# Optimization experiments

Measured on AMD Instinct MI355X. Metric: run time of the kernel, lower is better.

## Reference

```python
import jax, jax.numpy as jnp
import numpy as np

TOTAL_NODES = 262144
NUM_GRAPHS = 1024
MAX_NODES = 512
D = 256


def setup_inputs() -> dict:
    key = jax.random.key(0)
    k1, k2 = jax.random.split(key)
    node_emb = jax.random.normal(k1, (TOTAL_NODES, D), dtype=jnp.float32)
    batch_idx = jnp.sort(jax.random.randint(k2, (TOTAL_NODES,), 0, NUM_GRAPHS, dtype=jnp.int64))
    return {"node_emb": node_emb, "batch_idx": batch_idx,
            "num_graphs": NUM_GRAPHS, "max_nodes": MAX_NODES}


def reference(node_emb, batch_idx, num_graphs, max_nodes):
    # counts[g] = number of nodes in graph g  (torch.bincount)
    n = node_emb.shape[0]
    counts = jax.ops.segment_sum(jnp.ones((n,), dtype=jnp.int32), batch_idx,
                                 num_segments=num_graphs)
    # exclusive prefix sum -> start offset of each graph's node block
    starts = jnp.cumsum(counts) - counts
    # position of each node within its graph (batch_idx is sorted)
    pos = jnp.arange(n, dtype=jnp.int32) - starts[batch_idx]
    # single fused scatter replacing the per-graph python loop
    enc_states = jnp.zeros((num_graphs, max_nodes, node_emb.shape[-1]),
                           dtype=node_emb.dtype)
    enc_states = enc_states.at[batch_idx, pos].set(node_emb)
    # mask: first counts[g] slots of each row are 1
    enc_mask = (jnp.arange(max_nodes, dtype=jnp.int32)[None, :]
                < counts[:, None]).astype(jnp.int32)
    return enc_states, enc_mask
```

## Files before the change

kernel.cpp:

```cpp
#include <hip/hip_runtime.h>

#define NUM_GRAPHS 1024
#define MAX_NODES  512
#define DIM        256
#define D4         (DIM / 4)

typedef float f4 __attribute__((ext_vector_type(4)));

__device__ __forceinline__ int lower_bound_idx(const int* __restrict__ b, int n,
                                               bool is64, int key) {
    int lo = 0, hi = n;
    while (lo < hi) {
        int mid = (lo + hi) >> 1;
        int v = is64 ? b[2 * mid] : b[mid];
        if (v < key) lo = mid + 1; else hi = mid;
    }
    return lo;
}

__global__ void __launch_bounds__(256)
scatter_states_kernel(const f4* __restrict__ emb,
                      const int* __restrict__ bidx32, int n,
                      f4* __restrict__ out, float* __restrict__ mask) {
    __shared__ int sc[2];
    const int g = blockIdx.x;

    if (threadIdx.x < 2) {
        const bool is64 = (bidx32[n - 1] == 0);
        sc[threadIdx.x] = lower_bound_idx(bidx32, n, is64, g + threadIdx.x);
    }
    __syncthreads();
    const int s = sc[0];
    const int c = sc[1] - sc[0];

    const int lane  = threadIdx.x & 63;
    const int w     = threadIdx.x >> 6;
    const int rbase = w * 128;

    const f4* wemb = emb + (size_t)(s + rbase) * D4 + lane;
    f4*       wout = out + ((size_t)g * MAX_NODES + rbase) * D4 + lane;

    int ncopy = c - rbase;
    ncopy = ncopy < 0 ? 0 : (ncopy > 128 ? 128 : ncopy);

    int it = 0;
#pragma unroll 8
    for (; it < ncopy; ++it)
        wout[it * D4] = wemb[it * D4];
    const f4 z = (f4)(0.f);
#pragma unroll 8
    for (; it < 128; ++it)
        wout[it * D4] = z;

    float* mg = mask + (size_t)g * MAX_NODES;
    mg[threadIdx.x]       = (threadIdx.x < c)       ? 1.0f : 0.0f;
    mg[256 + threadIdx.x] = (256 + (int)threadIdx.x < c) ? 1.0f : 0.0f;
}

extern "C" void kernel_launch(void* const* d_in, const int* in_sizes, int n_in,
                              void* d_out, int out_size, void* d_ws, size_t ws_size,
                              hipStream_t stream) {
    const float* node_emb = (const float*)d_in[0];
    const int*   bidx32   = (const int*)d_in[1];
    const int    n        = in_sizes[1];

    float* mask = (float*)d_out + (size_t)NUM_GRAPHS * MAX_NODES * DIM;
    scatter_states_kernel<<<NUM_GRAPHS, 256, 0, stream>>>(
        (const f4*)node_emb, bidx32, n, (f4*)d_out, mask);
}
```

Baseline: 173.5 us.

## Assign one wavefront per graph and compute segment bounds per wave

Each 64-lane wavefront now handles one whole graph (all 512 rows) instead of a block of four waves splitting rows. Each wave runs its own binary search, with lanes alternating between the start and end keys, and broadcasts the bounds via shuffles, removing the shared memory and block barrier. The grid shrinks to a quarter as many blocks. This cuts per-block synchronisation and serial search latency, but each wave now does a longer serial copy loop of 512 rows and the work per wave becomes less balanced.

```diff
diff --git a/kernel.cpp b/kernel.cpp
--- a/kernel.cpp
+++ b/kernel.cpp
@@ -7,54 +7,44 @@
 
 typedef float f4 __attribute__((ext_vector_type(4)));
 
-__device__ __forceinline__ int lower_bound_idx(const int* __restrict__ b, int n,
-                                               bool is64, int key) {
-    int lo = 0, hi = n;
-    while (lo < hi) {
-        int mid = (lo + hi) >> 1;
-        int v = is64 ? b[2 * mid] : b[mid];
-        if (v < key) lo = mid + 1; else hi = mid;
-    }
-    return lo;
-}
-
 __global__ void __launch_bounds__(256)
 scatter_states_kernel(const f4* __restrict__ emb,
                       const int* __restrict__ bidx32, int n,
                       f4* __restrict__ out, float* __restrict__ mask) {
-    __shared__ int sc[2];
-    const int g = blockIdx.x;
+    const int lane = threadIdx.x & 63;
+    const int g    = (blockIdx.x * blockDim.x + threadIdx.x) >> 6;
 
-    if (threadIdx.x < 2) {
-        const bool is64 = (bidx32[n - 1] == 0);
-        sc[threadIdx.x] = lower_bound_idx(bidx32, n, is64, g + threadIdx.x);
+    const bool is64 = (bidx32[n - 1] == 0);
+
+    const int key = g + (lane & 1);
+    int lo = 0, hi = n;
+    while (lo < hi) {
+        int mid = (lo + hi) >> 1;
+        int v = is64 ? bidx32[2 * mid] : bidx32[mid];
+        if (v < key) lo = mid + 1; else hi = mid;
     }
-    __syncthreads();
-    const int s = sc[0];
-    const int c = sc[1] - sc[0];
+    const int s = __shfl(lo, 0, 64);
+    const int e = __shfl(lo, 1, 64);
+    const int c = e - s;
 
-    const int lane  = threadIdx.x & 63;
-    const int w     = threadIdx.x >> 6;
-    const int rbase = w * 128;
-
-    const f4* wemb = emb + (size_t)(s + rbase) * D4 + lane;
-    f4*       wout = out + ((size_t)g * MAX_NODES + rbase) * D4 + lane;
-
-    int ncopy = c - rbase;
-    ncopy = ncopy < 0 ? 0 : (ncopy > 128 ? 128 : ncopy);
+    const f4* wemb = emb + (size_t)s * D4 + lane;
+    f4*       wout = out + (size_t)g * MAX_NODES * D4 + lane;
 
     int it = 0;
 #pragma unroll 8
-    for (; it < ncopy; ++it)
+    for (; it < c; ++it)
         wout[it * D4] = wemb[it * D4];
     const f4 z = (f4)(0.f);
 #pragma unroll 8
-    for (; it < 128; ++it)
+    for (; it < MAX_NODES; ++it)
         wout[it * D4] = z;
 
     float* mg = mask + (size_t)g * MAX_NODES;
-    mg[threadIdx.x]       = (threadIdx.x < c)       ? 1.0f : 0.0f;
-    mg[256 + threadIdx.x] = (256 + (int)threadIdx.x < c) ? 1.0f : 0.0f;
+#pragma unroll
+    for (int k = 0; k < 8; ++k) {
+        const int slot = k * 64 + lane;
+        mg[slot] = (slot < c) ? 1.0f : 0.0f;
+    }
 }
 
 extern "C" void kernel_launch(void* const* d_in, const int* in_sizes, int n_in,
@@ -65,6 +55,6 @@
     const int    n        = in_sizes[1];
 
     float* mask = (float*)d_out + (size_t)NUM_GRAPHS * MAX_NODES * DIM;
-    scatter_states_kernel<<<NUM_GRAPHS, 256, 0, stream>>>(
+    scatter_states_kernel<<<NUM_GRAPHS / 4, 256, 0, stream>>>(
         (const f4*)node_emb, bidx32, n, (f4*)d_out, mask);
 }
```

New measurement: 179.0 us. +3.2%, slower.

## Split copy and zero-fill into separate kernels with balanced per-wave rows

Applied to the files above, without the earlier changes.

Replaces the single scatter kernel with two launches: one that copies each graph's rows and one that zero-fills the padding and writes the mask. Within each kernel, rows are now split evenly across the four waves instead of each wave owning a fixed 128-row slice. The aim is to stop waves whose slice holds no data from sitting idle or doing only zero stores, which should even out the load. In exchange it adds a second launch and repeats the binary search for each graph's bounds in both kernels.

```diff
diff --git a/kernel.cpp b/kernel.cpp
--- a/kernel.cpp
+++ b/kernel.cpp
@@ -18,42 +18,63 @@
     return lo;
 }
 
-__global__ void __launch_bounds__(256)
-scatter_states_kernel(const f4* __restrict__ emb,
-                      const int* __restrict__ bidx32, int n,
-                      f4* __restrict__ out, float* __restrict__ mask) {
-    __shared__ int sc[2];
-    const int g = blockIdx.x;
-
+__device__ __forceinline__ void block_meta(const int* __restrict__ bidx32, int n,
+                                           int g, int* sc) {
     if (threadIdx.x < 2) {
         const bool is64 = (bidx32[n - 1] == 0);
         sc[threadIdx.x] = lower_bound_idx(bidx32, n, is64, g + threadIdx.x);
     }
     __syncthreads();
+}
+
+
+__global__ void __launch_bounds__(256)
+copy_kernel(const f4* __restrict__ emb, const int* __restrict__ bidx32, int n,
+            f4* __restrict__ out) {
+    __shared__ int sc[2];
+    const int g = blockIdx.x;
+    block_meta(bidx32, n, g, sc);
     const int s = sc[0];
     const int c = sc[1] - sc[0];
 
-    const int lane  = threadIdx.x & 63;
-    const int w     = threadIdx.x >> 6;
-    const int rbase = w * 128;
+    const int lane = threadIdx.x & 63;
+    const int w    = threadIdx.x >> 6;
+    const int q    = (c + 3) >> 2;
+    const int r0   = min(w * q, c);
+    const int r1   = min(r0 + q, c);
 
-    const f4* wemb = emb + (size_t)(s + rbase) * D4 + lane;
-    f4*       wout = out + ((size_t)g * MAX_NODES + rbase) * D4 + lane;
+    const f4* wemb = emb + (size_t)(s + r0) * D4 + lane;
+    f4*       wout = out + ((size_t)g * MAX_NODES + r0) * D4 + lane;
+    const int cnt  = r1 - r0;
+#pragma unroll 8
+    for (int it = 0; it < cnt; ++it)
+        wout[it * D4] = wemb[it * D4];
+}
 
-    int ncopy = c - rbase;
-    ncopy = ncopy < 0 ? 0 : (ncopy > 128 ? 128 : ncopy);
+__global__ void __launch_bounds__(256)
+fill_kernel(const int* __restrict__ bidx32, int n,
+            f4* __restrict__ out, float* __restrict__ mask) {
+    __shared__ int sc[2];
+    const int g = blockIdx.x;
+    block_meta(bidx32, n, g, sc);
+    const int c   = sc[1] - sc[0];
+    const int pad = MAX_NODES - c;
 
-    int it = 0;
-#pragma unroll 8
-    for (; it < ncopy; ++it)
-        wout[it * D4] = wemb[it * D4];
+    const int lane = threadIdx.x & 63;
+    const int w    = threadIdx.x >> 6;
+    const int q    = (pad + 3) >> 2;
+    const int r0   = min(w * q, pad);
+    const int r1   = min(r0 + q, pad);
+
+    f4* wout = out + ((size_t)g * MAX_NODES + c + r0) * D4 + lane;
+    const int cnt = r1 - r0;
     const f4 z = (f4)(0.f);
 #pragma unroll 8
-    for (; it < 128; ++it)
+    for (int it = 0; it < cnt; ++it)
         wout[it * D4] = z;
 
     float* mg = mask + (size_t)g * MAX_NODES;
-    mg[threadIdx.x]       = (threadIdx.x < c)       ? 1.0f : 0.0f;
+    mg[threadIdx.x]       = ((int)threadIdx.x < c)       ? 1.0f : 0.0f;
     mg[256 + threadIdx.x] = (256 + (int)threadIdx.x < c) ? 1.0f : 0.0f;
 }
 
@@ -65,6 +86,9 @@
     const int    n        = in_sizes[1];
 
     float* mask = (float*)d_out + (size_t)NUM_GRAPHS * MAX_NODES * DIM;
-    scatter_states_kernel<<<NUM_GRAPHS, 256, 0, stream>>>(
-        (const f4*)node_emb, bidx32, n, (f4*)d_out, mask);
+
+    copy_kernel<<<NUM_GRAPHS, 256, 0, stream>>>(
+        (const f4*)node_emb, bidx32, n, (f4*)d_out);
+    fill_kernel<<<NUM_GRAPHS, 256, 0, stream>>>(
+        bidx32, n, (f4*)d_out, mask);
 }
```

Result: slower. 181.5 us (+4.6%).
